# Kernel optimization log

Measured on AMD Instinct MI355X. Metric: run time of the kernel, lower is better.

The kernel has to match this reference:

```python
import jax, jax.numpy as jnp
import numpy as np

B, L, N, DM = 32, 12, 883, 64
DSP, DTP, H, HID, HOR = 128, 128, 4, 64, 12
E_SPA = 14128
ENC_LAYERS = 3
HIDDEN = 5 * HID  # 2*embed + node + tid + diw = 320


def _gat(x, es, et, W, a_s, a_d, bias, edge_att=None):
    # GATConv-style attention with optional per-edge info-bottleneck mask (gat_ib)
    n = x.shape[0]
    h = (x @ W).reshape(n, H, -1)            # [n,H,Dh]
    sc_s = (h * a_s).sum(-1)                 # [n,H]
    sc_d = (h * a_d).sum(-1)
    al = jax.nn.leaky_relu(sc_s[es] + sc_d[et], 0.2)   # [E,H]
    al = al - jax.ops.segment_max(al, et, num_segments=n)[et]
    ex = jnp.exp(al)
    a = ex / jax.ops.segment_sum(ex, et, num_segments=n)[et]
    if edge_att is not None:
        a = a * edge_att[:, None]
    out = jax.ops.segment_sum(a[..., None] * h[es], et, num_segments=n)
    return out.reshape(n, -1) + bias


def _gsat(x, ei, gat_p, ext_p):
    # GSAT: embed -> extractor MLP on edge endpoint pairs -> sigmoid edge att -> masked conv
    es, et = ei[0], ei[1]
    emb = _gat(x, es, et, *gat_p)
    w1, b1, w2, b2, w3, b3 = ext_p
    f = jnp.concatenate([emb[es], emb[et]], axis=-1)
    logit = (jax.nn.relu(jax.nn.relu(f @ w1 + b1) @ w2 + b2) @ w3 + b3)[:, 0]
    att = jax.nn.sigmoid(logit)  # eval-mode (no concrete-relaxation sampling)
    return _gat(x, es, et, *gat_p, edge_att=att)


def setup_inputs():
    key = jax.random.key(0)
    ks = iter(jax.random.split(key, 80))
    def nrm(shape, s=0.02):
        return jax.random.normal(next(ks), shape, jnp.float32) * s
    hist = jax.random.normal(next(ks), (B, L, N, 3), jnp.float32)
    tid = jax.random.randint(next(ks), (B, L, N), 0, 288).astype(jnp.float32)
    diw = jax.random.randint(next(ks), (B, L, N), 0, 7).astype(jnp.float32)
    hist = hist.at[..., 1].set(tid).at[..., 2].set(diw)
    ei_spa = jax.random.randint(next(ks), (2, E_SPA), 0, N).astype(jnp.int32)
    g = jnp.arange(L, dtype=jnp.int32)
    ei_temp = jnp.stack([jnp.repeat(g, L), jnp.tile(g, L)])  # dense lag x lag temporal graph
    inp = dict(history_data=hist, edge_idx_spa=ei_spa, edge_idx_temp=ei_temp)
    inp.update(
        node_emb=nrm((N, HID)), tid_emb=nrm((288, HID)), diw_emb=nrm((7, HID)),
        start_w=nrm((3, DM)), start_b=jnp.zeros((DM,), jnp.float32),
        ts_w=nrm((DM * L, HID)), ts_b=jnp.zeros((HID,), jnp.float32),
        tr_spat_w=nrm((L * DM, DSP)), tr_spat_b=jnp.zeros((DSP,), jnp.float32),
        inv_spat_w=nrm((DSP, L * DM)), inv_spat_b=jnp.zeros((L * DM,), jnp.float32),
        tr_temp_w=nrm((N * DM, DTP)), tr_temp_b=jnp.zeros((DTP,), jnp.float32),
        inv_temp_w=nrm((DTP, N * DM)), inv_temp_b=jnp.zeros((N * DM,), jnp.float32),
        gat_sp_w=nrm((DSP, DSP)), gat_sp_asrc=nrm((H, DSP // H)), gat_sp_adst=nrm((H, DSP // H)), gat_sp_bias=jnp.zeros((DSP,), jnp.float32),
        ext_sp_w1=nrm((2 * DSP, 4 * DSP)), ext_sp_b1=jnp.zeros((4 * DSP,), jnp.float32),
        ext_sp_w2=nrm((4 * DSP, DSP)), ext_sp_b2=jnp.zeros((DSP,), jnp.float32),
        ext_sp_w3=nrm((DSP, 1)), ext_sp_b3=jnp.zeros((1,), jnp.float32),
        gat_tp_w=nrm((DTP, DTP)), gat_tp_asrc=nrm((H, DTP // H)), gat_tp_adst=nrm((H, DTP // H)), gat_tp_bias=jnp.zeros((DTP,), jnp.float32),
        ext_tp_w1=nrm((2 * DTP, 4 * DTP)), ext_tp_b1=jnp.zeros((4 * DTP,), jnp.float32),
        ext_tp_w2=nrm((4 * DTP, DTP)), ext_tp_b2=jnp.zeros((DTP,), jnp.float32),
        ext_tp_w3=nrm((DTP, 1)), ext_tp_b3=jnp.zeros((1,), jnp.float32),
        enc_w1=nrm((ENC_LAYERS, HIDDEN, HIDDEN)), enc_b1=jnp.zeros((ENC_LAYERS, HIDDEN), jnp.float32),
        enc_w2=nrm((ENC_LAYERS, HIDDEN, HIDDEN)), enc_b2=jnp.zeros((ENC_LAYERS, HIDDEN), jnp.float32),
        reg_w=nrm((HIDDEN, HOR)), reg_b=jnp.zeros((HOR,), jnp.float32),
    )
    return inp


def reference(history_data, edge_idx_spa, edge_idx_temp, node_emb, tid_emb, diw_emb,
              start_w, start_b, ts_w, ts_b,
              tr_spat_w, tr_spat_b, inv_spat_w, inv_spat_b,
              tr_temp_w, tr_temp_b, inv_temp_w, inv_temp_b,
              gat_sp_w, gat_sp_asrc, gat_sp_adst, gat_sp_bias,
              ext_sp_w1, ext_sp_b1, ext_sp_w2, ext_sp_b2, ext_sp_w3, ext_sp_b3,
              gat_tp_w, gat_tp_asrc, gat_tp_adst, gat_tp_bias,
              ext_tp_w1, ext_tp_b1, ext_tp_w2, ext_tp_b2, ext_tp_w3, ext_tp_b3,
              enc_w1, enc_b1, enc_w2, enc_b2, reg_w, reg_b):
    b, l, n = history_data.shape[:3]
    tid = jax.lax.stop_gradient(history_data[:, -1, :, 1]).astype(jnp.int32)
    diw = jax.lax.stop_gradient(history_data[:, -1, :, 2]).astype(jnp.int32)
    X = history_data[..., :3] @ start_w + start_b           # [B,L,N,DM]
    res = X.transpose(0, 2, 1, 3).reshape(b, n, l * DM)      # [B,N,L*DM]
    ts_res = res @ ts_w + ts_b                               # conv1x1 over nodes == per-node linear
    gp_sp = (gat_sp_w, gat_sp_asrc, gat_sp_adst, gat_sp_bias)
    ep_sp = (ext_sp_w1, ext_sp_b1, ext_sp_w2, ext_sp_b2, ext_sp_w3, ext_sp_b3)
    gp_tp = (gat_tp_w, gat_tp_asrc, gat_tp_adst, gat_tp_bias)
    ep_tp = (ext_tp_w1, ext_tp_b1, ext_tp_w2, ext_tp_b2, ext_tp_w3, ext_tp_b3)
    # batch_st_gsat: per-sample spatial GSAT then temporal GSAT (vmapped instead of Python loop)
    spa_in = res @ tr_spat_w + tr_spat_b                     # [B,N,DSP]
    spa_out = jax.vmap(lambda xx: _gsat(xx, edge_idx_spa, gp_sp, ep_sp))(spa_in)
    spa_back = (spa_out @ inv_spat_w + inv_spat_b).reshape(b, n, l, DM).transpose(0, 2, 1, 3)
    temp_in = spa_back.reshape(b, l, n * DM) @ tr_temp_w + tr_temp_b   # [B,L,DTP]
    temp_out = jax.vmap(lambda xx: _gsat(xx, edge_idx_temp, gp_tp, ep_tp))(temp_in)
    temp_back = (temp_out @ inv_temp_w + inv_temp_b).reshape(b, l, n, DM)
    ts_temp = temp_back.transpose(0, 2, 1, 3).reshape(b, n, l * DM) @ ts_w + ts_b
    hid = jnp.concatenate([
        ts_res, ts_temp,
        jnp.broadcast_to(node_emb, (b, n, HID)),
        tid_emb[tid], diw_emb[diw],
    ], axis=-1)                                              # [B,N,320]
    for i in range(ENC_LAYERS):  # MLP_res: x + fc2(relu(fc1(x)))
        hid = hid + jax.nn.relu(hid @ enc_w1[i] + enc_b1[i]) @ enc_w2[i] + enc_b2[i]
    pred = hid @ reg_w + reg_b                               # [B,N,HOR]
    return pred.transpose(0, 2, 1)[..., None]                # [B,HOR,N,1]
```

## Files before the change

kernel.cpp:

```cpp
#include <hip/hip_runtime.h>
#include <hip/hip_bf16.h>
#include <cstdint>
#include <cstddef>

#define B_   32
#define L_   12
#define N_   883
#define DM_  64
#define E_SP 14128
#define E_TP 144
#define NT_  12
#define RBN  28256
#define RBL  384
#define LDM  768
#define NDM  56512

static inline int cdiv_h(int a, int b){ return (a+b-1)/b; }

__device__ __forceinline__ ushort f2bf(float f){
    unsigned u = __float_as_uint(f);
    unsigned lsb = (u >> 16) & 1u;
    u += 0x7fffu + lsb;
    return (ushort)(u >> 16);
}
__device__ __forceinline__ float bf2f(ushort h){
    return __uint_as_float(((unsigned)h) << 16);
}
__device__ __forceinline__ ushort f2h(float f){
    _Float16 h = (_Float16)f;
    ushort r; __builtin_memcpy(&r, &h, 2);
    return r;
}

typedef __bf16 bf16x8 __attribute__((ext_vector_type(8)));
typedef _Float16 f16x8 __attribute__((ext_vector_type(8)));
typedef _Float16 f16x2 __attribute__((ext_vector_type(2)));
typedef float  f32x4  __attribute__((ext_vector_type(4)));
typedef short  s16x2  __attribute__((ext_vector_type(2)));
union BF8 { bf16x8 v; ushort u[8]; unsigned w[4]; int4 i; };
union HF8 { f16x8 v; ushort u[8]; unsigned w[4]; int4 i; };

__device__ __forceinline__ unsigned pkrelu(unsigned x){
    s16x2 v;
    __builtin_memcpy(&v, &x, 4);
    s16x2 z = 0;
    v = __builtin_elementwise_max(v, z);
    unsigned r;
    __builtin_memcpy(&r, &v, 4);
    return r;
}
__device__ __forceinline__ unsigned pkaddh(unsigned x, unsigned y){
    f16x2 a, b;
    __builtin_memcpy(&a, &x, 4);
    __builtin_memcpy(&b, &y, 4);
    a = a + b;
    unsigned r;
    __builtin_memcpy(&r, &a, 4);
    return r;
}

__global__ void k_mkA(const float* __restrict__ sw, const float* __restrict__ sb,
                      const float* __restrict__ tsw, const float* __restrict__ tsb,
                      const float* __restrict__ trsp, const float* __restrict__ trspb,
                      float* __restrict__ A1, float* __restrict__ A2,
                      float* __restrict__ cb1, float* __restrict__ cb2)
{
    int idx = blockIdx.x*256 + threadIdx.x;
    if (idx < 36*64) {
        int k = idx >> 6, h = idx & 63;
        int l = k/3, c = k - l*3;
        float s = 0.f;
        #pragma unroll 8
        for (int d = 0; d < 64; ++d) s += sw[c*64+d]*tsw[(size_t)(l*64+d)*64 + h];
        A1[idx] = s;
    } else if (idx < 36*64 + 36*128) {
        int i = idx - 36*64;
        int k = i >> 7, p = i & 127;
        int l = k/3, c = k - l*3;
        float s = 0.f;
        #pragma unroll 8
        for (int d = 0; d < 64; ++d) s += sw[c*64+d]*trsp[(size_t)(l*64+d)*128 + p];
        A2[i] = s;
    } else if (idx < 36*64 + 36*128 + 64) {
        int h = idx - (36*64 + 36*128);
        float s = tsb[h];
        #pragma unroll 8
        for (int k = 0; k < 768; ++k) s += sb[k & 63]*tsw[(size_t)k*64 + h];
        cb1[h] = s;
    } else if (idx < 36*64 + 36*128 + 64 + 128) {
        int p = idx - (36*64 + 36*128 + 64);
        float s = trspb[p];
        #pragma unroll 8
        for (int k = 0; k < 768; ++k) s += sb[k & 63]*trsp[(size_t)k*128 + p];
        cb2[p] = s;
    }
}
__global__ void k_front(const float* __restrict__ hist, const float* __restrict__ A1,
                        const float* __restrict__ A2, const float* __restrict__ cb1,
                        const float* __restrict__ cb2, float* __restrict__ ts_res,
                        ushort* __restrict__ spa_in)
{
    int idx = blockIdx.x*256 + threadIdx.x;
    if (idx >= RBN*192) return;
    int bn = idx / 192, h = idx - bn*192;
    int b = bn / N_, n = bn - b*N_;
    const float* hp = hist + ((size_t)(b*L_)*N_ + n)*3;
    bool isTs = (h < 64);
    int hh = isTs ? h : (h - 64);
    int stride = isTs ? 64 : 128;
    const float* A = isTs ? (A1 + hh) : (A2 + hh);
    float acc = isTs ? cb1[hh] : cb2[hh];
    #pragma unroll
    for (int l = 0; l < 12; ++l) {
        float x0 = hp[l*2649 + 0];
        float x1 = hp[l*2649 + 1];
        float x2 = hp[l*2649 + 2];
        acc += x0*A[(l*3+0)*stride] + x1*A[(l*3+1)*stride] + x2*A[(l*3+2)*stride];
    }
    if (isTs) ts_res[(size_t)bn*64 + hh] = acc;
    else      spa_in[(size_t)bn*128 + hh] = f2bf(acc);
}

template<int CT, int AMODE, int EPI, bool RELU, bool RES>
__launch_bounds__(256)
__global__ void mgemm(const ushort* __restrict__ A, const ushort* __restrict__ WT,
                      const float* __restrict__ bias, float* __restrict__ resF,
                      void* __restrict__ outP, int M, int N, int K)
{
    const int t = threadIdx.x, wv = t >> 6, l = t & 63;
    const int lr = l & 15, lk = l >> 4;
    const int row0 = blockIdx.y*64 + wv*16;
    const int col0 = blockIdx.x * (CT*16);
    int arr = row0 + lr; if (arr >= M) arr = M-1;
    int ab = 0, an = 0;
    if (AMODE == 1) { ab = arr / N_; an = arr - ab*N_; }
    const ushort* ap = A + (size_t)arr*K + lk*8;
    f32x4 acc[CT] = {};
    for (int k0 = 0; k0 < K; k0 += 32) {
        BF8 af;
        if (AMODE == 0) af.i = *(const int4*)(ap + k0);
        else {
            int k = k0 + lk*8; int ll = k >> 6, d = k & 63;
            af.i = *(const int4*)(A + ((size_t)(ab*L_ + ll))*NDM + (size_t)an*64 + d);
        }
        #pragma unroll
        for (int ct = 0; ct < CT; ++ct) {
            BF8 bf; bf.i = *(const int4*)&WT[(size_t)(col0 + ct*16 + lr)*K + k0 + lk*8];
            acc[ct] = __builtin_amdgcn_mfma_f32_16x16x32_bf16(af.v, bf.v, acc[ct], 0, 0, 0);
        }
    }
    #pragma unroll
    for (int ct = 0; ct < CT; ++ct) {
        int c = col0 + ct*16 + lr;
        float bv = 0.f;
        if (EPI == 2) { if (bias && c < 12) bv = bias[c]; }
        else if (bias) bv = bias[c];
        #pragma unroll
        for (int g = 0; g < 4; ++g) {
            int r = row0 + lk*4 + g;
            if (r >= M) continue;
            float v = acc[ct][g] + bv;
            if (RELU) v = fmaxf(v, 0.f);
            if (RES) {
                v += resF[(size_t)r*N + c];
                resF[(size_t)r*N + c] = v;
            }
            if (EPI == 0) {
                ((ushort*)outP)[(size_t)r*N + c] = f2bf(v);
            } else if (EPI == 1) {
                ((float*)outP)[(size_t)r*N + c] = v;
            } else if (EPI == 2) {
                if (c < 12) {
                    int b = r / N_, n = r - (r/N_)*N_;
                    ((float*)outP)[((size_t)(b*L_ + c))*N_ + n] = v;
                }
            } else {
                int b = r / N_, n = r - (r/N_)*N_;
                ((ushort*)outP)[((size_t)(b*L_ + (c>>6)))*NDM + (size_t)n*64 + (c&63)] = f2bf(v);
            }
        }
    }
}

template<int RT, int CT, int EPI, bool RELU, bool RES>
__launch_bounds__(256)
__global__ void mgemm_rt(const ushort* __restrict__ A, const ushort* __restrict__ WT,
                         const float* __restrict__ bias, float* __restrict__ resF,
                         void* __restrict__ outP, int M, int N, int K)
{
    const int t = threadIdx.x, wv = t >> 6, l = t & 63;
    const int lr = l & 15, lk = l >> 4;
    const int rowbase = blockIdx.y*(4*RT*16) + wv*(RT*16);
    const int col0 = blockIdx.x * (CT*16);
    const ushort* ap[RT];
    #pragma unroll
    for (int rt = 0; rt < RT; ++rt) {
        int arr = rowbase + rt*16 + lr; if (arr >= M) arr = M-1;
        ap[rt] = A + (size_t)arr*K + lk*8;
    }
    f32x4 acc[RT][CT] = {};
    for (int k0 = 0; k0 < K; k0 += 32) {
        BF8 af[RT];
        #pragma unroll
        for (int rt = 0; rt < RT; ++rt) af[rt].i = *(const int4*)(ap[rt] + k0);
        #pragma unroll
        for (int ct = 0; ct < CT; ++ct) {
            BF8 bf; bf.i = *(const int4*)&WT[(size_t)(col0 + ct*16 + lr)*K + k0 + lk*8];
            #pragma unroll
            for (int rt = 0; rt < RT; ++rt)
                acc[rt][ct] = __builtin_amdgcn_mfma_f32_16x16x32_bf16(af[rt].v, bf.v,
                                                                     acc[rt][ct], 0, 0, 0);
        }
    }
    #pragma unroll
    for (int rt = 0; rt < RT; ++rt)
        #pragma unroll
        for (int ct = 0; ct < CT; ++ct) {
            int c = col0 + ct*16 + lr;
            float bv = bias ? bias[c] : 0.f;
            #pragma unroll
            for (int g = 0; g < 4; ++g) {
                int r = rowbase + rt*16 + lk*4 + g;
                if (r >= M) continue;
                float v = acc[rt][ct][g] + bv;
                if (RELU) v = fmaxf(v, 0.f);
                if (RES) {
                    v += resF[(size_t)r*N + c];
                    resF[(size_t)r*N + c] = v;
                }
                if (EPI == 0) {
                    ((ushort*)outP)[(size_t)r*N + c] = f2bf(v);
                } else if (EPI == 1) {
                    ((float*)outP)[(size_t)r*N + c] = v;
                } else if (EPI == 4) {
                    ((ushort*)outP)[(size_t)r*N + c] = f2h(v);
                } else {
                    int b = r / N_, n = r - (r/N_)*N_;
                    ((ushort*)outP)[((size_t)(b*L_ + (c>>6)))*NDM + (size_t)n*64 + (c&63)] = f2bf(v);
                }
            }
        }
}

#define TCH 1024
__launch_bounds__(256)
__global__ void temp_in_mfma(const ushort* __restrict__ AT, const ushort* __restrict__ WtT,
                             float* __restrict__ out)
{
    const int t = threadIdx.x, wv = t >> 6, l = t & 63;
    const int lr = l & 15, lk = l >> 4;
    const int row0 = blockIdx.y * 96;
    const int c0 = wv * 32;
    const int k0b = blockIdx.x * TCH;
    const int kend = (k0b + TCH < NDM) ? (k0b + TCH) : NDM;
    f32x4 acc[6][2] = {};
    for (int k0 = k0b; k0 < kend; k0 += 32) {
        BF8 b0, b1;
        b0.i = *(const int4*)&WtT[(size_t)(c0 + lr)*NDM + k0 + lk*8];
        b1.i = *(const int4*)&WtT[(size_t)(c0 + 16 + lr)*NDM + k0 + lk*8];
        #pragma unroll
        for (int m = 0; m < 6; ++m) {
            BF8 af; af.i = *(const int4*)&AT[(size_t)(row0 + m*16 + lr)*NDM + k0 + lk*8];
            acc[m][0] = __builtin_amdgcn_mfma_f32_16x16x32_bf16(af.v, b0.v, acc[m][0], 0, 0, 0);
            acc[m][1] = __builtin_amdgcn_mfma_f32_16x16x32_bf16(af.v, b1.v, acc[m][1], 0, 0, 0);
        }
    }
    #pragma unroll
    for (int m = 0; m < 6; ++m)
        #pragma unroll
        for (int ct = 0; ct < 2; ++ct) {
            int c = c0 + ct*16 + lr;
            #pragma unroll
            for (int g = 0; g < 4; ++g) {
                int r = row0 + m*16 + lk*4 + g;
                atomicAdd(&out[(size_t)r*128 + c], acc[m][ct][g]);
            }
        }
}

__global__ void k_sc(const ushort* __restrict__ h, const float* __restrict__ as_,
                     const float* __restrict__ ad_, float* __restrict__ scs,
                     float* __restrict__ scd, int R)
{
    int r = blockIdx.x*256 + threadIdx.x;
    if (r >= R) return;
    const ushort* hr = h + (size_t)r*128;
    #pragma unroll
    for (int hh = 0; hh < 4; ++hh) {
        float ss = 0.f, sd = 0.f;
        #pragma unroll
        for (int k = 0; k < 32; ++k) {
            float hv = bf2f(hr[hh*32 + k]);
            ss += hv*as_[hh*32+k];
            sd += hv*ad_[hh*32+k];
        }
        scs[(size_t)r*4+hh] = ss;
        scd[(size_t)r*4+hh] = sd;
    }
}

__global__ void k_count(const int* __restrict__ ei, int E, int* __restrict__ counts){
    int e = blockIdx.x*256 + threadIdx.x;
    if (e < E) atomicAdd(&counts[ei[E + e]], 1);
}
__global__ void k_scan(const int* __restrict__ counts, int* __restrict__ off,
                       int* __restrict__ cur, int n)
{
    __shared__ int s[1024];
    int t = threadIdx.x;
    int v0 = (t < n) ? counts[t] : 0;
    s[t] = v0;
    __syncthreads();
    for (int o = 1; o < 1024; o <<= 1) {
        int v = (t >= o) ? s[t-o] : 0;
        __syncthreads();
        s[t] += v;
        __syncthreads();
    }
    if (t < n) {
        off[t+1] = s[t];
        cur[t] = s[t] - v0;
        if (t == 0) off[0] = 0;
    }
}
__global__ void k_fill(const int* __restrict__ ei, int E, int* __restrict__ cur,
                       int* __restrict__ lst){
    int e = blockIdx.x*256 + threadIdx.x;
    if (e < E) {
        int pos = atomicAdd(&cur[ei[E+e]], 1);
        lst[pos] = e;
    }
}

template<bool USE_ATT>
__global__ void k_gather(const ushort* __restrict__ h, const float* __restrict__ scs,
                         const float* __restrict__ scd, const float* __restrict__ att,
                         const int* __restrict__ ei, const int* __restrict__ off,
                         const int* __restrict__ lst, const float* __restrict__ bias,
                         ushort* __restrict__ out, int E, int NN)
{
    int bn = blockIdx.x*4 + (threadIdx.x >> 6);
    int b = bn / NN, n = bn - b*NN;
    int lane = threadIdx.x & 63;
    int c0 = lane*2;
    int hh = lane >> 4;
    float sd = scd[(size_t)bn*4 + hh];
    int o0 = off[n], o1 = off[n+1];
    float ax = 0.f, ay = 0.f, sa = 0.f;
    for (int i = o0; i < o1; ++i) {
        int e = lst[i];
        int s = ei[e];
        float al = scs[(size_t)(b*NN + s)*4 + hh] + sd;
        al = al > 0.f ? al : 0.2f*al;
        float ex = expf(al);
        sa += ex;
        float a = USE_ATT ? ex * att[(size_t)b*E + e] : ex;
        unsigned hv = *(const unsigned*)&h[((size_t)b*NN + s)*128 + c0];
        ax += a * __uint_as_float(hv << 16);
        ay += a * __uint_as_float(hv & 0xffff0000u);
    }
    float rn = (sa > 0.f) ? 1.f/sa : 0.f;
    ushort2 o2;
    o2.x = f2bf(ax*rn + bias[c0]);
    o2.y = f2bf(ay*rn + bias[c0+1]);
    *(ushort2*)&out[(size_t)bn*128 + c0] = o2;
}

__global__ void k_prepW2(const float* __restrict__ W2, ushort* __restrict__ W2T)
{
    int idx = blockIdx.x*256 + threadIdx.x;
    if (idx >= 512*128) return;
    int k = idx >> 7, c = idx & 127;
    W2T[(size_t)c*512 + k] = f2h(W2[idx]);
}
__global__ void k_prepT(const float* __restrict__ W, ushort* __restrict__ WT, int K, int N)
{
    int idx = blockIdx.x*256 + threadIdx.x;
    if (idx >= K*N) return;
    int k = idx / N, c = idx - k*N;
    WT[(size_t)c*K + k] = f2bf(W[idx]);
}
__global__ void k_prepWtT(const float* __restrict__ W, ushort* __restrict__ WT)
{
    __shared__ ushort tile[128][129];
    int k0 = blockIdx.x * 128;
    int t = threadIdx.x;
    for (int i = t; i < 128*128; i += 256) {
        int k = i >> 7, c = i & 127;
        int kk = k0 + k;
        tile[c][k] = (kk < NDM) ? f2bf(W[(size_t)kk*128 + c]) : (ushort)0;
    }
    __syncthreads();
    for (int i = t; i < 128*128; i += 256) {
        int c = i >> 7, k = i & 127;
        int kk = k0 + k;
        if (kk < NDM) WT[(size_t)c*NDM + kk] = tile[c][k];
    }
}
__global__ void k_prepT_big(const float* __restrict__ W, ushort* __restrict__ WT)
{
    __shared__ float tile[128][65];
    int c0 = blockIdx.x * 64;
    int t = threadIdx.x;
    for (int i = t; i < 128*64; i += 256) {
        int k = i >> 6, ci = i & 63;
        tile[k][ci] = W[(size_t)k*NDM + c0 + ci];
    }
    __syncthreads();
    for (int i = t; i < 64*128; i += 256) {
        int ci = i >> 7, k = i & 127;
        WT[(size_t)(c0 + ci)*128 + k] = f2bf(tile[k][ci]);
    }
}
__global__ void k_bcat(const float* __restrict__ b1, float* __restrict__ dst){
    int i = blockIdx.x*256 + threadIdx.x;
    if (i < 1024) dst[i] = (i < 512) ? b1[i] : 0.f;
}

template<bool SWZ>
__launch_bounds__(256, 3)
__global__ void ext2_mfma(const ushort* __restrict__ PQ, const ushort* __restrict__ W2T,
                          const float* __restrict__ b2, const float* __restrict__ w3,
                          const float* __restrict__ b3p, const int* __restrict__ ei,
                          const int* __restrict__ lst,
                          float* __restrict__ att, int E, int NN, int nblk)
{
    __shared__ ushort Bs[2][128*40];
    int bid = blockIdx.x;
    if (SWZ) {
        bid = (blockIdx.x & 7) * (gridDim.x >> 3) + (blockIdx.x >> 3);
        if (bid >= nblk) bid = nblk - 1;
    }
    const int t = threadIdx.x;
    const int wv = t >> 6, l = t & 63;
    const int lr = l & 15, lk = l >> 4;

    const ushort* pr[2]; const ushort* qr[2];
    int row0[2];
    #pragma unroll
    for (int rt = 0; rt < 2; ++rt) {
        row0[rt] = bid*128 + wv*32 + rt*16;
        int r = row0[rt] + lr;
        int b = (int)((unsigned)r / (unsigned)E), i = r - b*E;
        int e = lst[i];
        pr[rt] = PQ + ((size_t)b*NN + ei[e])*1024 + lk*8;
        qr[rt] = PQ + ((size_t)b*NN + ei[E+e])*1024 + 512 + lk*8;
    }
    const int sc = t >> 1, sh = (t & 1) * 16;
    const ushort* wsrc = W2T + (size_t)sc*512 + sh;
    ushort* wd0 = &Bs[0][sc*40 + sh];
    ushort* wd1 = &Bs[1][sc*40 + sh];

    {
        int4 a0 = *(const int4*)(wsrc);
        int4 a1 = *(const int4*)(wsrc + 8);
        *(int4*)wd0 = a0;
        *(int4*)(wd0 + 8) = a1;
    }
    HF8 pu[2], qu[2];
    #pragma unroll
    for (int rt = 0; rt < 2; ++rt) {
        pu[rt].i = *(const int4*)(pr[rt]);
        qu[rt].i = *(const int4*)(qr[rt]);
    }
    int4 bnA = *(const int4*)(wsrc + 32);
    int4 bnB = *(const int4*)(wsrc + 40);
    __syncthreads();

    f32x4 acc[2][8] = {};
    for (int kc = 0; kc < 16; ++kc) {
        const int cb = kc & 1;
        HF8 af[2];
        #pragma unroll
        for (int rt = 0; rt < 2; ++rt)
            #pragma unroll
            for (int j = 0; j < 4; ++j)
                af[rt].w[j] = pkrelu(pkaddh(pu[rt].w[j], qu[rt].w[j]));
        {
            int ka = (kc+1 < 15) ? kc+1 : 15;
            #pragma unroll
            for (int rt = 0; rt < 2; ++rt) {
                pu[rt].i = *(const int4*)(pr[rt] + ka*32);
                qu[rt].i = *(const int4*)(qr[rt] + ka*32);
            }
        }
        __builtin_amdgcn_s_setprio(1);
        #pragma unroll
        for (int ct = 0; ct < 8; ++ct) {
            HF8 bfm;
            bfm.v = *(const f16x8*)&Bs[cb][(ct*16 + lr)*40 + lk*8];
            #pragma unroll
            for (int rt = 0; rt < 2; ++rt)
                acc[rt][ct] = __builtin_amdgcn_mfma_f32_16x16x32_f16(af[rt].v, bfm.v,
                                                                    acc[rt][ct], 0, 0, 0);
        }
        __builtin_amdgcn_s_setprio(0);
        if (kc < 15) {
            ushort* wd = cb ? wd0 : wd1;
            *(int4*)wd = bnA;
            *(int4*)(wd + 8) = bnB;
        }
        {
            int kb = (kc+2 < 15) ? kc+2 : 15;
            bnA = *(const int4*)(wsrc + kb*32);
            bnB = *(const int4*)(wsrc + kb*32 + 8);
        }
        __syncthreads();
    }
    float b3 = b3p[0];
    #pragma unroll
    for (int rt = 0; rt < 2; ++rt) {
        float part[4] = {0.f,0.f,0.f,0.f};
        #pragma unroll
        for (int ct = 0; ct < 8; ++ct) {
            int c = ct*16 + lr;
            float b2v = b2[c], w3v = w3[c];
            #pragma unroll
            for (int g = 0; g < 4; ++g)
                part[g] += fmaxf(acc[rt][ct][g] + b2v, 0.f) * w3v;
        }
        #pragma unroll
        for (int m = 1; m < 16; m <<= 1)
            #pragma unroll
            for (int g = 0; g < 4; ++g)
                part[g] += __shfl_xor(part[g], m, 64);
        if (lr == 0) {
            #pragma unroll
            for (int g = 0; g < 4; ++g) {
                int rr = row0[rt] + lk*4 + g;
                int b = (int)((unsigned)rr / (unsigned)E), i = rr - b*E;
                int e = lst[i];
                att[(size_t)b*E + e] = 1.f/(1.f + expf(-(part[g] + b3)));
            }
        }
    }
}

__global__ void k_bias_fill(float* __restrict__ dst, const float* __restrict__ bias, int n){
    int i = blockIdx.x*256 + threadIdx.x;
    if (i < n) dst[i] = bias[i & 127];
}
__global__ void k_f2b(const float* __restrict__ src, ushort* __restrict__ dst, int n){
    int i = blockIdx.x*256 + threadIdx.x;
    if (i < n) dst[i] = f2bf(src[i]);
}

__global__ void k_hid(const float* __restrict__ ts_res, const float* __restrict__ ts_temp,
                      const float* __restrict__ node_emb, const float* __restrict__ tid_emb,
                      const float* __restrict__ diw_emb, const float* __restrict__ hist,
                      float* __restrict__ hid, ushort* __restrict__ hidB)
{
    int idx = blockIdx.x*256 + threadIdx.x;
    if (idx >= RBN*320) return;
    int r = idx / 320, c = idx - r*320;
    int b = r / N_, n = r - b*N_;
    float v;
    if (c < 64)        v = ts_res[(size_t)r*64 + c];
    else if (c < 128)  v = ts_temp[(size_t)r*64 + (c-64)];
    else if (c < 192)  v = node_emb[(size_t)n*64 + (c-128)];
    else if (c < 256) {
        int tid = (int)hist[((size_t)(b*L_ + (L_-1))*N_ + n)*3 + 1];
        v = tid_emb[(size_t)tid*64 + (c-192)];
    } else {
        int diw = (int)hist[((size_t)(b*L_ + (L_-1))*N_ + n)*3 + 2];
        v = diw_emb[(size_t)diw*64 + (c-256)];
    }
    hid[idx] = v;
    hidB[idx] = f2bf(v);
}

extern "C" void kernel_launch(void* const* d_in, const int* in_sizes, int n_in,
                              void* d_out, int out_size, void* d_ws, size_t ws_size,
                              hipStream_t stream)
{
    (void)in_sizes; (void)n_in; (void)out_size; (void)ws_size;
    const float* hist      = (const float*)d_in[0];
    const int*   ei_sp     = (const int*)  d_in[1];
    const int*   ei_tp     = (const int*)  d_in[2];
    const float* node_emb  = (const float*)d_in[3];
    const float* tid_emb   = (const float*)d_in[4];
    const float* diw_emb   = (const float*)d_in[5];
    const float* start_w   = (const float*)d_in[6];
    const float* start_b   = (const float*)d_in[7];
    const float* ts_w      = (const float*)d_in[8];
    const float* ts_b      = (const float*)d_in[9];
    const float* tr_spat_w = (const float*)d_in[10];
    const float* tr_spat_b = (const float*)d_in[11];
    const float* inv_spat_w= (const float*)d_in[12];
    const float* inv_spat_b= (const float*)d_in[13];
    const float* tr_temp_w = (const float*)d_in[14];
    const float* tr_temp_b = (const float*)d_in[15];
    const float* inv_temp_w= (const float*)d_in[16];
    const float* inv_temp_b= (const float*)d_in[17];
    const float* gat_sp_w  = (const float*)d_in[18];
    const float* gat_sp_as = (const float*)d_in[19];
    const float* gat_sp_ad = (const float*)d_in[20];
    const float* gat_sp_b  = (const float*)d_in[21];
    const float* ext_sp_w1 = (const float*)d_in[22];
    const float* ext_sp_b1 = (const float*)d_in[23];
    const float* ext_sp_w2 = (const float*)d_in[24];
    const float* ext_sp_b2 = (const float*)d_in[25];
    const float* ext_sp_w3 = (const float*)d_in[26];
    const float* ext_sp_b3 = (const float*)d_in[27];
    const float* gat_tp_w  = (const float*)d_in[28];
    const float* gat_tp_as = (const float*)d_in[29];
    const float* gat_tp_ad = (const float*)d_in[30];
    const float* gat_tp_b  = (const float*)d_in[31];
    const float* ext_tp_w1 = (const float*)d_in[32];
    const float* ext_tp_b1 = (const float*)d_in[33];
    const float* ext_tp_w2 = (const float*)d_in[34];
    const float* ext_tp_b2 = (const float*)d_in[35];
    const float* ext_tp_w3 = (const float*)d_in[36];
    const float* ext_tp_b3 = (const float*)d_in[37];
    const float* enc_w1    = (const float*)d_in[38];
    const float* enc_b1    = (const float*)d_in[39];
    const float* enc_w2    = (const float*)d_in[40];
    const float* enc_b2    = (const float*)d_in[41];
    const float* reg_w     = (const float*)d_in[42];
    const float* reg_b     = (const float*)d_in[43];
    float* out = (float*)d_out;

    size_t o = 0;
    char* wsb = (char*)d_ws;
    auto allocB = [&](size_t bytes) -> void* {
        void* p = wsb + o;
        o += (bytes + 255) & ~(size_t)255;
        return p;
    };
    void* bufA = allocB((size_t)RBN*768*2);
    void* bufB = allocB((size_t)RBN*768*2);
    void* bufC = allocB((size_t)RBN*512*2);
    void* bufD = allocB((size_t)RBN*320*2);
    float*  ts_res  = (float*)allocB((size_t)RBN*64*4);
    ushort* spaB    = (ushort*)allocB((size_t)RBN*128*2);
    ushort* hB      = (ushort*)allocB((size_t)RBN*128*2);
    float*  sc_s    = (float*)allocB((size_t)RBN*4*4);
    float*  sc_d    = (float*)allocB((size_t)RBN*4*4);
    float*  att     = (float*)allocB((size_t)B_*E_SP*4);
    ushort* embB    = (ushort*)allocB((size_t)RBN*128*2);
    int*    csr     = (int*)allocB(17024*4);
    float*  temp_in = (float*)allocB((size_t)RBL*128*4);
    ushort* tempB   = (ushort*)allocB((size_t)RBL*128*2);
    ushort* toutB   = (ushort*)allocB((size_t)RBL*128*2);
    ushort* PQ_t    = (ushort*)allocB((size_t)RBL*1024*2);
    float*  ts_temp = (float*)allocB((size_t)RBN*64*4);
    ushort* W2T_sp  = (ushort*)allocB(512*128*2);
    ushort* W2T_tp  = (ushort*)allocB(512*128*2);
    ushort* WtT     = (ushort*)allocB((size_t)128*NDM*2);
    ushort* itWT    = (ushort*)allocB((size_t)NDM*128*2);
    ushort* ispWT   = (ushort*)allocB(768*128*2);
    ushort* gspWT   = (ushort*)allocB(128*128*2);
    ushort* gtpWT   = (ushort*)allocB(128*128*2);
    ushort* w1catT_sp = (ushort*)allocB((size_t)1024*128*2);
    ushort* w1catT_tp = (ushort*)allocB((size_t)1024*128*2);
    float*  b1cat_sp  = (float*)allocB(1024*4);
    float*  b1cat_tp  = (float*)allocB(1024*4);
    ushort* w1T_enc = (ushort*)allocB((size_t)3*320*320*2);
    ushort* w2T_enc = (ushort*)allocB((size_t)3*320*320*2);
    ushort* tswT_hi = (ushort*)allocB(64*768*2);
    ushort* reg_wT  = (ushort*)allocB(16*320*2);
    float*  A1      = (float*)allocB(36*64*4);
    float*  A2      = (float*)allocB(36*128*4);
    float*  cb1     = (float*)allocB(64*4);
    float*  cb2     = (float*)allocB(128*4);

    ushort* AT    = (ushort*)bufA;
    float*  hid   = (float*)bufA;
    ushort* PQ_sp = (ushort*)bufB;
    ushort* tback = (ushort*)bufB;
    ushort* hidB  = (ushort*)bufC;
    ushort* R1b   = (ushort*)bufD;

    int* counts_sp = csr;
    int* off_sp    = csr + 883;
    int* cur_sp    = csr + 1767;
    int* list_sp   = csr + 2650;
    int* counts_tp = csr + 16778;
    int* off_tp    = csr + 16790;
    int* cur_tp    = csr + 16803;
    int* list_tp   = csr + 16815;

    hipMemsetAsync(counts_sp, 0, 883*4, stream);
    k_count<<<cdiv_h(E_SP,256),256,0,stream>>>(ei_sp, E_SP, counts_sp);
    k_scan<<<1,1024,0,stream>>>(counts_sp, off_sp, cur_sp, 883);
    k_fill<<<cdiv_h(E_SP,256),256,0,stream>>>(ei_sp, E_SP, cur_sp, list_sp);
    hipMemsetAsync(counts_tp, 0, 12*4, stream);
    k_count<<<1,256,0,stream>>>(ei_tp, E_TP, counts_tp);
    k_scan<<<1,1024,0,stream>>>(counts_tp, off_tp, cur_tp, 12);
    k_fill<<<1,256,0,stream>>>(ei_tp, E_TP, cur_tp, list_tp);
    k_mkA<<<cdiv_h(36*64+36*128+192,256),256,0,stream>>>(start_w, start_b, ts_w, ts_b,
                                                         tr_spat_w, tr_spat_b,
                                                         A1, A2, cb1, cb2);
    k_prepW2<<<cdiv_h(512*128,256),256,0,stream>>>(ext_sp_w2, W2T_sp);
    k_prepW2<<<cdiv_h(512*128,256),256,0,stream>>>(ext_tp_w2, W2T_tp);
    k_prepWtT<<<cdiv_h(NDM,128),256,0,stream>>>(tr_temp_w, WtT);
    k_prepT_big<<<NDM/64,256,0,stream>>>(inv_temp_w, itWT);
    k_prepT<<<cdiv_h(128*768,256),256,0,stream>>>(inv_spat_w, ispWT, 128, 768);
    k_prepT<<<cdiv_h(128*128,256),256,0,stream>>>(gat_sp_w, gspWT, 128, 128);
    k_prepT<<<cdiv_h(128*128,256),256,0,stream>>>(gat_tp_w, gtpWT, 128, 128);
    k_prepT<<<cdiv_h(128*512,256),256,0,stream>>>(ext_sp_w1,           w1catT_sp,           128, 512);
    k_prepT<<<cdiv_h(128*512,256),256,0,stream>>>(ext_sp_w1 + 128*512, w1catT_sp + 512*128, 128, 512);
    k_prepT<<<cdiv_h(128*512,256),256,0,stream>>>(ext_tp_w1,           w1catT_tp,           128, 512);
    k_prepT<<<cdiv_h(128*512,256),256,0,stream>>>(ext_tp_w1 + 128*512, w1catT_tp + 512*128, 128, 512);
    k_bcat<<<4,256,0,stream>>>(ext_sp_b1, b1cat_sp);
    k_bcat<<<4,256,0,stream>>>(ext_tp_b1, b1cat_tp);
    for (int i = 0; i < 3; ++i) {
        k_prepT<<<cdiv_h(320*320,256),256,0,stream>>>(enc_w1 + (size_t)i*320*320, w1T_enc + (size_t)i*320*320, 320, 320);
        k_prepT<<<cdiv_h(320*320,256),256,0,stream>>>(enc_w2 + (size_t)i*320*320, w2T_enc + (size_t)i*320*320, 320, 320);
    }
    k_prepT<<<cdiv_h(768*64,256),256,0,stream>>>(ts_w, tswT_hi, 768, 64);
    hipMemsetAsync(reg_wT, 0, 16*320*2, stream);
    k_prepT<<<cdiv_h(320*12,256),256,0,stream>>>(reg_w, reg_wT, 320, 12);

    k_front<<<cdiv_h(RBN*192,256),256,0,stream>>>(hist, A1, A2, cb1, cb2, ts_res, spaB);

    mgemm_rt<2,4,0,false,false><<<dim3(2,221),256,0,stream>>>(spaB, gspWT, nullptr, nullptr,
                                                              hB, RBN, 128, 128);
    k_sc<<<cdiv_h(RBN,256),256,0,stream>>>(hB, gat_sp_as, gat_sp_ad, sc_s, sc_d, RBN);
    k_gather<false><<<RBN/4,256,0,stream>>>(hB, sc_s, sc_d, nullptr, ei_sp, off_sp, list_sp,
                                            gat_sp_b, embB, E_SP, N_);
    mgemm_rt<2,8,4,false,false><<<dim3(8,221),256,0,stream>>>(embB, w1catT_sp, b1cat_sp, nullptr,
                                                              PQ_sp, RBN, 1024, 128);
    ext2_mfma<true><<<3536,256,0,stream>>>(PQ_sp, W2T_sp, ext_sp_b2, ext_sp_w3, ext_sp_b3,
                                           ei_sp, list_sp, att, E_SP, N_, (B_*E_SP)/128);
    k_gather<true><<<RBN/4,256,0,stream>>>(hB, sc_s, sc_d, att, ei_sp, off_sp, list_sp,
                                           gat_sp_b, spaB, E_SP, N_);

    mgemm_rt<2,4,3,false,false><<<dim3(12,221),256,0,stream>>>(spaB, ispWT, inv_spat_b, nullptr,
                                                               AT, RBN, 768, 128);
    k_bias_fill<<<cdiv_h(RBL*128,256),256,0,stream>>>(temp_in, tr_temp_b, RBL*128);
    temp_in_mfma<<<dim3(56,4),256,0,stream>>>(AT, WtT, temp_in);
    k_f2b<<<cdiv_h(RBL*128,256),256,0,stream>>>(temp_in, tempB, RBL*128);

    mgemm_rt<2,4,0,false,false><<<dim3(2,3),256,0,stream>>>(tempB, gtpWT, nullptr, nullptr,
                                                            hB, RBL, 128, 128);
    k_sc<<<cdiv_h(RBL,256),256,0,stream>>>(hB, gat_tp_as, gat_tp_ad, sc_s, sc_d, RBL);
    k_gather<false><<<RBL/4,256,0,stream>>>(hB, sc_s, sc_d, nullptr, ei_tp, off_tp, list_tp,
                                            gat_tp_b, embB, E_TP, NT_);
    mgemm_rt<2,8,4,false,false><<<dim3(8,3),256,0,stream>>>(embB, w1catT_tp, b1cat_tp, nullptr,
                                                            PQ_t, RBL, 1024, 128);
    ext2_mfma<false><<<(B_*E_TP)/128,256,0,stream>>>(PQ_t, W2T_tp, ext_tp_b2, ext_tp_w3,
                                                     ext_tp_b3, ei_tp, list_tp, att, E_TP, NT_,
                                                     (B_*E_TP)/128);
    k_gather<true><<<RBL/4,256,0,stream>>>(hB, sc_s, sc_d, att, ei_tp, off_tp, list_tp,
                                           gat_tp_b, toutB, E_TP, NT_);

    mgemm_rt<2,4,0,false,false><<<dim3(883,3),256,0,stream>>>(toutB, itWT, inv_temp_b, nullptr,
                                                              tback, RBL, NDM, 128);
    mgemm<4,1,1,false,false><<<dim3(1,442),256,0,stream>>>(tback, tswT_hi, ts_b, nullptr,
                                                           ts_temp, RBN, 64, LDM);

    k_hid<<<cdiv_h(RBN*320,256),256,0,stream>>>(ts_res, ts_temp, node_emb, tid_emb, diw_emb, hist,
                                                hid, hidB);
    for (int i = 0; i < 3; ++i) {
        mgemm_rt<2,5,0,true,false><<<dim3(4,221),256,0,stream>>>(hidB, w1T_enc + (size_t)i*320*320,
                                                                 enc_b1 + i*320, nullptr, R1b, RBN, 320, 320);
        mgemm_rt<2,5,0,false,true><<<dim3(4,221),256,0,stream>>>(R1b, w2T_enc + (size_t)i*320*320,
                                                                 enc_b2 + i*320, hid, hidB, RBN, 320, 320);
    }
    mgemm<1,0,2,false,false><<<dim3(1,442),256,0,stream>>>(hidB, reg_wT, reg_b, nullptr,
                                                           out, RBN, 16, 320);
}
```

Measured before the change: 1.281 ms.

## Fuse inverse temporal projection and ts_temp GEMM into one per-node kernel

```diff
diff --git a/kernel.cpp b/kernel.cpp
--- a/kernel.cpp
+++ b/kernel.cpp
@@ -276,6 +276,73 @@
                 atomicAdd(&out[(size_t)r*128 + c], acc[m][ct][g]);
             }
         }
+}
+
+__launch_bounds__(256)
+__global__ void k_tsTemp(const ushort* __restrict__ toutB, const ushort* __restrict__ itWT,
+                         const float* __restrict__ itb, const ushort* __restrict__ tswT,
+                         const float* __restrict__ tsb, float* __restrict__ ts_temp)
+{
+    __shared__ ushort sb[384*72];
+    const int n = blockIdx.x;
+    const int t = threadIdx.x, wv = t >> 6, l = t & 63;
+    const int lr = l & 15, lk = l >> 4;
+    {
+        f32x4 acc1[6][4] = {};
+        for (int k0 = 0; k0 < 128; k0 += 32) {
+            BF8 bfr[4];
+            #pragma unroll
+            for (int ct = 0; ct < 4; ++ct)
+                bfr[ct].i = *(const int4*)&itWT[(size_t)(n*64 + ct*16 + lr)*128 + k0 + lk*8];
+            #pragma unroll
+            for (int rt = 0; rt < 6; ++rt) {
+                BF8 af; af.i = *(const int4*)&toutB[(size_t)(wv*96 + rt*16 + lr)*128 + k0 + lk*8];
+                #pragma unroll
+                for (int ct = 0; ct < 4; ++ct)
+                    acc1[rt][ct] = __builtin_amdgcn_mfma_f32_16x16x32_bf16(af.v, bfr[ct].v,
+                                                                          acc1[rt][ct], 0, 0, 0);
+            }
+        }
+        #pragma unroll
+        for (int rt = 0; rt < 6; ++rt)
+            #pragma unroll
+            for (int ct = 0; ct < 4; ++ct) {
+                int d = ct*16 + lr;
+                float bv = itb[n*64 + d];
+                #pragma unroll
+                for (int g = 0; g < 4; ++g) {
+                    int r = wv*96 + rt*16 + lk*4 + g;
+                    int bb = r / 12;
+                    sb[r*72 + (d ^ ((bb & 7) << 3))] = f2bf(acc1[rt][ct][g] + bv);
+                }
+            }
+    }
+    __syncthreads();
+    f32x4 acc2[2] = {};
+    #pragma unroll 2
+    for (int j = 0; j < 24; ++j) {
+        BF8 bfm; bfm.i = *(const int4*)&tswT[(size_t)(wv*16 + lr)*768 + j*32 + lk*8];
+        int lidx = j >> 1;
+        int koff = (j & 1)*32 + lk*8;
+        #pragma unroll
+        for (int rt = 0; rt < 2; ++rt) {
+            int bb = rt*16 + lr;
+            BF8 af;
+            af.v = *(const bf16x8*)&sb[(bb*12 + lidx)*72 + (koff ^ ((bb & 7) << 3))];
+            acc2[rt] = __builtin_amdgcn_mfma_f32_16x16x32_bf16(af.v, bfm.v, acc2[rt], 0, 0, 0);
+        }
+    }
+    {
+        int h = wv*16 + lr;
+        float bv = tsb[h];
+        #pragma unroll
+        for (int rt = 0; rt < 2; ++rt)
+            #pragma unroll
+            for (int g = 0; g < 4; ++g) {
+                int bb = rt*16 + lk*4 + g;
+                ts_temp[((size_t)bb*N_ + n)*64 + h] = acc2[rt][g] + bv;
+            }
+    }
 }
 
 __global__ void k_sc(const ushort* __restrict__ h, const float* __restrict__ as_,
@@ -667,7 +734,6 @@
     ushort* AT    = (ushort*)bufA;
     float*  hid   = (float*)bufA;
     ushort* PQ_sp = (ushort*)bufB;
-    ushort* tback = (ushort*)bufB;
     ushort* hidB  = (ushort*)bufC;
     ushort* R1b   = (ushort*)bufD;
 
@@ -745,10 +811,7 @@
     k_gather<true><<<RBL/4,256,0,stream>>>(hB, sc_s, sc_d, att, ei_tp, off_tp, list_tp,
                                            gat_tp_b, toutB, E_TP, NT_);
 
-    mgemm_rt<2,4,0,false,false><<<dim3(883,3),256,0,stream>>>(toutB, itWT, inv_temp_b, nullptr,
-                                                              tback, RBL, NDM, 128);
-    mgemm<4,1,1,false,false><<<dim3(1,442),256,0,stream>>>(tback, tswT_hi, ts_b, nullptr,
-                                                           ts_temp, RBN, 64, LDM);
+    k_tsTemp<<<N_,256,0,stream>>>(toutB, itWT, inv_temp_b, tswT_hi, ts_b, ts_temp);
 
     k_hid<<<cdiv_h(RBN*320,256),256,0,stream>>>(ts_res, ts_temp, node_emb, tid_emb, diw_emb, hist,
                                                 hid, hidB);
```

New measurement: 1.232 ms. -3.9%, faster.
